# Performance work log

Measured on AMD Instinct MI355X. Metric: run time of the kernel, lower is better.

Reference implementation:

```python
import jax, jax.numpy as jnp
import numpy as np

B, S, D = 2, 2048, 2048
NQ, NKV = 32, 8
HD = D // NQ  # 64
THETA = 10000.0


def _rope_tables(seq_len, head_dim, theta):
    k = jnp.arange(0, head_dim, 2)[: head_dim // 2].astype(jnp.float32)
    inv_freq = 1.0 / (theta ** (k / head_dim))
    pos = jnp.arange(seq_len, dtype=jnp.float32)
    ang = pos[:, None] * inv_freq[None, :]          # [S, HD/2]
    ang = jnp.concatenate([ang, ang], axis=-1)       # [S, HD]
    return jnp.cos(ang), jnp.sin(ang)


def _apply_rope(x, cos, sin):
    # x: [B, H, S, HD]; cos/sin: [S, HD]
    h = x.shape[-1] // 2
    x1, x2 = x[..., :h], x[..., h:]
    rotated = jnp.concatenate([-x2, x1], axis=-1)
    return (x * cos[None, None] + rotated * sin[None, None]).astype(x.dtype)


def setup_inputs() -> dict:
    key = jax.random.key(0)
    ks = jax.random.split(key, 6)
    x = jax.random.normal(ks[0], (B, S, D), dtype=jnp.float32)
    attention_mask = jnp.ones((B, S), dtype=jnp.int32)
    Wq = jax.random.normal(ks[1], (NQ * HD, D), dtype=jnp.float32) * 0.02
    Wk = jax.random.normal(ks[2], (NKV * HD, D), dtype=jnp.float32) * 0.02
    Wv = jax.random.normal(ks[3], (NKV * HD, D), dtype=jnp.float32) * 0.02
    Wo = jax.random.normal(ks[4], (D, D), dtype=jnp.float32) * 0.02
    return {"x": x, "attention_mask": attention_mask,
            "Wq": Wq, "Wk": Wk, "Wv": Wv, "Wo": Wo}


def reference(x, attention_mask, Wq, Wk, Wv, Wo):
    b, s, d = x.shape
    # projections (nn.Linear: y = x @ W.T)
    q = jnp.einsum('bsd,od->bso', x, Wq).reshape(b, s, NQ, HD).transpose(0, 2, 1, 3)
    k = jnp.einsum('bsd,od->bso', x, Wk).reshape(b, s, NKV, HD).transpose(0, 2, 1, 3)
    v = jnp.einsum('bsd,od->bso', x, Wv).reshape(b, s, NKV, HD).transpose(0, 2, 1, 3)
    cos, sin = _rope_tables(s, HD, THETA)
    q = _apply_rope(q, cos, sin)
    k = _apply_rope(k, cos, sin)
    g = NQ // NKV
    k = jnp.repeat(k, g, axis=1)  # [b, NQ, s, HD]
    v = jnp.repeat(v, g, axis=1)
    attn = jnp.einsum('bhqd,bhkd->bhqk', q, k)
    causal = jnp.triu(jnp.ones((s, s), dtype=bool), k=1)
    attn = jnp.where(causal[None, None], -jnp.inf, attn)
    attn = jax.nn.softmax(attn / jnp.sqrt(jnp.float32(HD)), axis=-1)
    out = jnp.einsum('bhqk,bhkd->bhqd', attn, v)
    out = out.transpose(0, 2, 1, 3).reshape(b, s, d)
    return jnp.einsum('bsd,od->bso', out, Wo)
```

## Files before the change

kernel.cpp:

```cpp
#include <hip/hip_runtime.h>

#define B_   2
#define S_   2048
#define D_   2048
#define NQ_  32
#define NKV_ 8
#define HD_  64

typedef unsigned short u16;
typedef __bf16 bf16x8 __attribute__((ext_vector_type(8)));
typedef __bf16 bf16x4 __attribute__((ext_vector_type(4)));
typedef short  s16x4  __attribute__((ext_vector_type(4)));
typedef float  f32x4  __attribute__((ext_vector_type(4)));

#define GLB __attribute__((address_space(1)))
#define LDS __attribute__((address_space(3)))

__device__ inline u16 f2b(float f){
  union { float f; unsigned u; } v; v.f = f;
  unsigned r = (v.u + 0x7fffu + ((v.u >> 16) & 1u)) >> 16;
  return (u16)r;
}

__device__ inline f32x4 mfma16(bf16x4 a, bf16x4 b, f32x4 c){
  union U { bf16x4 b; s16x4 s; };
  U ua, ub; ua.b = a; ub.b = b;
  return __builtin_amdgcn_mfma_f32_16x16x16bf16_1k(ua.s, ub.s, c, 0, 0, 0);
}

__device__ inline bf16x4 pack4(float p0, float p1, float p2, float p3){
  union { float f; unsigned u; } a, b, c, d;
  a.f = p0; b.f = p1; c.f = p2; d.f = p3;
  union { uint2 u; bf16x4 v; } r;
  r.u.x = (a.u >> 16) | (b.u & 0xffff0000u);
  r.u.y = (c.u >> 16) | (d.u & 0xffff0000u);
  return r.v;
}

__global__ void k_f2b_all(const float* __restrict__ x,  const float* __restrict__ wq,
                          const float* __restrict__ wk, const float* __restrict__ wv,
                          const float* __restrict__ wo,
                          u16* __restrict__ xb, u16* __restrict__ wqkvb, u16* __restrict__ wob){
  int i = blockIdx.x * blockDim.x + threadIdx.x;
  const float* src; u16* dst; int off;
  if (i < 2097152)      { src = x;  dst = xb;                  off = i; }
  else if (i < 3145728) { src = wq; dst = wqkvb;               off = i - 2097152; }
  else if (i < 3407872) { src = wk; dst = wqkvb + 2048*2048;   off = i - 3145728; }
  else if (i < 3670016) { src = wv; dst = wqkvb + 2560*2048;   off = i - 3407872; }
  else                  { src = wo; dst = wob;                 off = i - 3670016; }
  float4 f = ((const float4*)src)[off];
  uint2 pk;
  pk.x = (unsigned)f2b(f.x) | ((unsigned)f2b(f.y) << 16);
  pk.y = (unsigned)f2b(f.z) | ((unsigned)f2b(f.w) << 16);
  ((uint2*)dst)[off] = pk;
}

#define GEMM_CORE(K)                                                           \
  __shared__ __align__(16) u16 As[128*64];                                     \
  __shared__ __align__(16) u16 Bs[128*64];                                     \
  const int tid  = threadIdx.x;                                               \
  const int lane = tid & 63;                                                  \
  const int wave = tid >> 6;                                                  \
  const int wm = wave >> 1, wn = wave & 1;                                    \
  const int quad = lane >> 4, l16 = lane & 15;                                \
  const u16* Ab = A  + (size_t)blockIdx.y * 128 * (K);                        \
  const u16* Bb = Bm + (size_t)blockIdx.x * 128 * (K);                        \
  f32x4 acc[4][4];                                                            \
  for (int i = 0; i < 4; i++)                                                 \
    for (int j = 0; j < 4; j++) acc[i][j] = (f32x4){0.f, 0.f, 0.f, 0.f};      \
  const int R0 = wave * 32;                                                   \
  const int lr = lane >> 3;                                                   \
  const int gc = ((lane & 7) ^ lr) * 8;                                       \
  const int sk = l16 & 7;                                                     \
  for (int k0 = 0; k0 < (K); k0 += 64){                                       \
    __syncthreads();                                                          \
    _Pragma("unroll")                                                         \
    for (int m = 0; m < 4; m++){                                              \
      const u16* ga = Ab + (size_t)(R0 + m*8 + lr) * (K) + k0 + gc;           \
      const u16* gb = Bb + (size_t)(R0 + m*8 + lr) * (K) + k0 + gc;           \
      __builtin_amdgcn_global_load_lds((const GLB void*)ga, (LDS void*)&As[(R0 + m*8)*64], 16, 0, 0); \
      __builtin_amdgcn_global_load_lds((const GLB void*)gb, (LDS void*)&Bs[(R0 + m*8)*64], 16, 0, 0); \
    }                                                                          \
    __syncthreads();                                                          \
    bf16x8 af[4][2], bfr[4][2];                                               \
    _Pragma("unroll")                                                         \
    for (int i = 0; i < 4; i++)                                               \
      _Pragma("unroll")                                                       \
      for (int h = 0; h < 2; h++)                                             \
        af[i][h]  = *(const bf16x8*)&As[(wm*64 + i*16 + l16)*64 + (((h*4 + quad) ^ sk)*8)]; \
    _Pragma("unroll")                                                         \
    for (int j = 0; j < 4; j++)                                               \
      _Pragma("unroll")                                                       \
      for (int h = 0; h < 2; h++)                                             \
        bfr[j][h] = *(const bf16x8*)&Bs[(wn*64 + j*16 + l16)*64 + (((h*4 + quad) ^ sk)*8)]; \
    _Pragma("unroll")                                                         \
    for (int i = 0; i < 4; i++)                                               \
      _Pragma("unroll")                                                       \
      for (int j = 0; j < 4; j++){                                            \
        acc[i][j] = __builtin_amdgcn_mfma_f32_16x16x32_bf16(af[i][0], bfr[j][0], acc[i][j], 0, 0, 0); \
        acc[i][j] = __builtin_amdgcn_mfma_f32_16x16x32_bf16(af[i][1], bfr[j][1], acc[i][j], 0, 0, 0); \
      }                                                                        \
  }

#define QSCALE 0.18033688011112042f
__global__ __launch_bounds__(256, 3) void k_gemm_qkv(const u16* __restrict__ A,
                                                     const u16* __restrict__ Bm,
                                                     u16* __restrict__ qT,
                                                     u16* __restrict__ kT,
                                                     u16* __restrict__ vT){
  GEMM_CORE(2048)

  const int cb = blockIdx.x*128 + wn*64;

  if (cb < 2560){
    const bool isq = (cb < 2048);
    const int hh   = (isq ? cb : (cb - 2048)) >> 6;
    const int NH   = isq ? NQ_ : NKV_;
    u16* base      = isq ? qT : kT;
    const float sc = isq ? QSCALE : 1.0f;
    #pragma unroll
    for (int j = 0; j < 2; j++){
      const int d2 = j*16 + l16;
      const float invf = __expf(-(float)d2 * (9.210340371976184f / 32.0f));
      #pragma unroll
      for (int i = 0; i < 4; i++){
        const int row0 = blockIdx.y*128 + wm*64 + i*16 + quad*4;
        #pragma unroll
        for (int r = 0; r < 4; r++){
          const int row = row0 + r;
          const int s = row & (S_ - 1), b = row >> 11;
          float ang = (float)s * invf;
          float sn = __sinf(ang), cs = __cosf(ang);
          const float x1 = acc[i][j][r] * sc, x2 = acc[i][j+2][r] * sc;
          u16* drow = base + ((size_t)(b*NH + hh) * S_ + s) * 64;
          drow[d2]      = f2b(x1*cs - x2*sn);
          drow[d2 + 32] = f2b(x2*cs + x1*sn);
        }
      }
    }
  } else {
    const int fbase = cb - 2560;
    #pragma unroll
    for (int j = 0; j < 4; j++){
      const int f = fbase + j*16 + l16;
      const int kvh = f >> 6, d = f & 63;
      #pragma unroll
      for (int i = 0; i < 4; i++){
        const int row0 = blockIdx.y*128 + wm*64 + i*16 + quad*4;
        const int s0 = row0 & (S_ - 1), b = row0 >> 11;
        uint2 pk;
        pk.x = (unsigned)f2b(acc[i][j][0]) | ((unsigned)f2b(acc[i][j][1]) << 16);
        pk.y = (unsigned)f2b(acc[i][j][2]) | ((unsigned)f2b(acc[i][j][3]) << 16);
        *(uint2*)(vT + ((size_t)(b*NKV_ + kvh) * 64 + d) * S_ + s0) = pk;
      }
    }
  }
}

__global__ __launch_bounds__(256, 3) void k_gemm_bt(const u16* __restrict__ A,
                                                    const u16* __restrict__ Bm,
                                                    float* __restrict__ C,
                                                    int N){
  GEMM_CORE(2048)
  for (int i = 0; i < 4; i++){
    int row0 = blockIdx.y*128 + wm*64 + i*16 + quad*4;
    for (int j = 0; j < 4; j++){
      int col = blockIdx.x*128 + wn*64 + j*16 + l16;
      for (int r = 0; r < 4; r++)
        C[(size_t)(row0 + r) * N + col] = acc[i][j][r];
    }
  }
}

__global__ __launch_bounds__(256) void k_attn(const u16* __restrict__ qT,
                                              const u16* __restrict__ kT,
                                              const u16* __restrict__ vT,
                                              u16* __restrict__ aout){
  __shared__ __align__(16) u16 Ks[2][64*64];
  __shared__ __align__(16) u16 Vs[2][64*64];

  const int bid = blockIdx.x;
  const int kvh = bid & 7;
  const int b   = (bid >> 3) & 1;
  const int hq  = (bid >> 4) & 3;
  const int T   = 15 - (bid >> 6);
  const int h   = kvh*4 + hq;
  const int lane = threadIdx.x & 63, w = threadIdx.x >> 6;
  const int quad = lane >> 4, l16 = lane & 15;

  const u16* Qh = qT + (size_t)(b*NQ_ + h)    * S_ * 64;
  const u16* Kh = kT + (size_t)(b*NKV_ + kvh) * S_ * 64;
  const u16* Vh = vT + (size_t)(b*NKV_ + kvh) * 64 * S_;

  const int rr = lane >> 3;
  const int gg = (lane & 7) ^ rr;
  const int R  = w * 16;

  auto stage = [&](int c, int buf){
    const int kb = c * 64;
    const u16* gk0 = Kh + (size_t)(kb + R + rr)     * 64 + gg*8;
    const u16* gk1 = Kh + (size_t)(kb + R + 8 + rr) * 64 + gg*8;
    const u16* gv0 = Vh + (size_t)(R + rr)     * S_ + kb + gg*8;
    const u16* gv1 = Vh + (size_t)(R + 8 + rr) * S_ + kb + gg*8;
    __builtin_amdgcn_global_load_lds((const GLB void*)gk0, (LDS void*)&Ks[buf][R*64],     16, 0, 0);
    __builtin_amdgcn_global_load_lds((const GLB void*)gk1, (LDS void*)&Ks[buf][(R+8)*64], 16, 0, 0);
    __builtin_amdgcn_global_load_lds((const GLB void*)gv0, (LDS void*)&Vs[buf][R*64],     16, 0, 0);
    __builtin_amdgcn_global_load_lds((const GLB void*)gv1, (LDS void*)&Vs[buf][(R+8)*64], 16, 0, 0);
  };

  const int sw    = l16 & 7;
  const int koff0 = ((quad    ) ^ sw) * 8;
  const int koff1 = ((quad + 4) ^ sw) * 8;
  int voff[4];
  #pragma unroll
  for (int t = 0; t < 4; t++)
    voff[t] = (((2*t + (quad >> 1)) ^ sw) * 8) + (quad & 1)*4;

  const int qb0 = 2*T, qb1 = 2*T + 1;
  const int qr0 = T*128 + w*16 + l16;
  const int qr1 = qr0 + 64;

  stage(0, 0);

  bf16x8 qf[2][2];
  qf[0][0] = *(const bf16x8*)(Qh + (size_t)qr0*64 + quad*8);
  qf[0][1] = *(const bf16x8*)(Qh + (size_t)qr0*64 + 32 + quad*8);
  qf[1][0] = *(const bf16x8*)(Qh + (size_t)qr1*64 + quad*8);
  qf[1][1] = *(const bf16x8*)(Qh + (size_t)qr1*64 + 32 + quad*8);

  f32x4 o[2][4];
  #pragma unroll
  for (int s = 0; s < 2; s++)
    for (int dt = 0; dt < 4; dt++) o[s][dt] = (f32x4){0.f, 0.f, 0.f, 0.f};
  float lrow[2] = {0.f, 0.f};

  for (int c = 0; c <= qb1; c++){
    const int buf = c & 1;
    __syncthreads();
    if (c < qb1) stage(c+1, buf^1);

    const bool act0  = (c <= qb0);
    const bool diag0 = (c == qb0);
    const bool diag1 = (c == qb1);
    const u16* Kb = &Ks[buf][0];
    const u16* Vb = &Vs[buf][0];

    bf16x4 pk[2][4];
    #pragma unroll
    for (int t = 0; t < 4; t++){
      const bool n0 = act0 && !(diag0 && t > w);
      const bool n1 = !(diag1 && t > w);
      if (!n0 && !n1) continue;
      const int rowb = (t*16 + l16)*64;
      bf16x8 ka0 = *(const bf16x8*)&Kb[rowb + koff0];
      bf16x8 ka1 = *(const bf16x8*)&Kb[rowb + koff1];
      #pragma unroll
      for (int s = 0; s < 2; s++){
        if (s == 0 ? !n0 : !n1) continue;
        f32x4 z = (f32x4){0.f, 0.f, 0.f, 0.f};
        z = __builtin_amdgcn_mfma_f32_16x16x32_bf16(ka0, qf[s][0], z, 0, 0, 0);
        z = __builtin_amdgcn_mfma_f32_16x16x32_bf16(ka1, qf[s][1], z, 0, 0, 0);
        if ((s == 0 ? diag0 : diag1) && t == w){
          #pragma unroll
          for (int r = 0; r < 4; r++)
            if (quad*4 + r > l16) z[r] = -1e30f;
        }
        float p0 = __builtin_amdgcn_exp2f(z[0]);
        float p1 = __builtin_amdgcn_exp2f(z[1]);
        float p2 = __builtin_amdgcn_exp2f(z[2]);
        float p3 = __builtin_amdgcn_exp2f(z[3]);
        lrow[s] += (p0 + p1) + (p2 + p3);
        pk[s][t] = pack4(p0, p1, p2, p3);
      }
    }

    #pragma unroll
    for (int dt = 0; dt < 4; dt++){
      const int rowb = (dt*16 + l16)*64;
      #pragma unroll
      for (int t = 0; t < 4; t++){
        const bool n0 = act0 && !(diag0 && t > w);
        const bool n1 = !(diag1 && t > w);
        if (!n0 && !n1) continue;
        bf16x4 va = *(const bf16x4*)&Vb[rowb + voff[t]];
        if (n0) o[0][dt] = mfma16(va, pk[0][t], o[0][dt]);
        if (n1) o[1][dt] = mfma16(va, pk[1][t], o[1][dt]);
      }
    }
  }

  #pragma unroll
  for (int s = 0; s < 2; s++){
    float lsum = lrow[s];
    lsum += __shfl_xor(lsum, 16, 64);
    lsum += __shfl_xor(lsum, 32, 64);
    float inv = 1.0f / lsum;
    const int qrow = s ? qr1 : qr0;
    u16* orow = aout + (size_t)(b*S_ + qrow) * D_ + h*64;
    #pragma unroll
    for (int dt = 0; dt < 4; dt++){
      uint2 pkd;
      u16 e0 = f2b(o[s][dt][0] * inv), e1 = f2b(o[s][dt][1] * inv);
      u16 e2 = f2b(o[s][dt][2] * inv), e3 = f2b(o[s][dt][3] * inv);
      pkd.x = (unsigned)e0 | ((unsigned)e1 << 16);
      pkd.y = (unsigned)e2 | ((unsigned)e3 << 16);
      *(uint2*)(orow + dt*16 + quad*4) = pkd;
    }
  }
}

extern "C" void kernel_launch(void* const* d_in, const int* in_sizes, int n_in,
                              void* d_out, int out_size, void* d_ws, size_t ws_size,
                              hipStream_t stream){
  const float* x  = (const float*)d_in[0];
  const float* Wq = (const float*)d_in[2];
  const float* Wk = (const float*)d_in[3];
  const float* Wv = (const float*)d_in[4];
  const float* Wo = (const float*)d_in[5];

  char* ws = (char*)d_ws;
  u16* xb    = (u16*)(ws);
  u16* wqkvb = (u16*)(ws + 16777216);
  u16* wob   = (u16*)(ws + 29360128);
  u16* qTp   = (u16*)(ws + 37748736);
  u16* kTp   = (u16*)(ws + 54525952);
  u16* vTp   = (u16*)(ws + 58720256);
  u16* attnOut = xb;

  k_f2b_all<<<dim3(18432), 256, 0, stream>>>(x, Wq, Wk, Wv, Wo, xb, wqkvb, wob);

  k_gemm_qkv<<<dim3(24, 32), 256, 0, stream>>>(xb, wqkvb, qTp, kTp, vTp);

  k_attn<<<dim3(1024), 256, 0, stream>>>(qTp, kTp, vTp, attnOut);

  k_gemm_bt<<<dim3(16, 32), 256, 0, stream>>>(attnOut, wob, (float*)d_out, 2048);
}
```

Baseline: 297.4 us.

## Split causal attention KV range across paired blocks and merge partials

Each attention block now handles two query tiles (p and 15-p), each over half of its KV range, so every block gets an equal amount of causal work. Unnormalized partial outputs and row sums go to two workspace buffers, and a new combine kernel sums them and normalizes. This removes the tail imbalance of the causal triangle but adds an extra kernel launch, extra global traffic for the bf16 partials, and an extra bf16 rounding step. It relies on the fixed-max exp2 trick (no running max), so partials can be added directly.

```diff
diff --git a/kernel.cpp b/kernel.cpp
--- a/kernel.cpp
+++ b/kernel.cpp
@@ -20,6 +20,10 @@
   union { float f; unsigned u; } v; v.f = f;
   unsigned r = (v.u + 0x7fffu + ((v.u >> 16) & 1u)) >> 16;
   return (u16)r;
+}
+__device__ inline float b2f(u16 b){
+  union { unsigned u; float f; } v; v.u = ((unsigned)b) << 16;
+  return v.f;
 }
 
 __device__ inline f32x4 mfma16(bf16x4 a, bf16x4 b, f32x4 c){
@@ -175,16 +179,20 @@
 __global__ __launch_bounds__(256) void k_attn(const u16* __restrict__ qT,
                                               const u16* __restrict__ kT,
                                               const u16* __restrict__ vT,
-                                              u16* __restrict__ aout){
+                                              u16* __restrict__ P1,
+                                              u16* __restrict__ P2,
+                                              float* __restrict__ l1,
+                                              float* __restrict__ l2){
   __shared__ __align__(16) u16 Ks[2][64*64];
   __shared__ __align__(16) u16 Vs[2][64*64];
 
-  const int bid = blockIdx.x;
-  const int kvh = bid & 7;
-  const int b   = (bid >> 3) & 1;
-  const int hq  = (bid >> 4) & 3;
-  const int T   = 15 - (bid >> 6);
-  const int h   = kvh*4 + hq;
+  const int bid  = blockIdx.x;
+  const int kvh  = bid & 7;
+  const int b    = (bid >> 3) & 1;
+  const int hq   = (bid >> 4) & 3;
+  const int p    = (bid >> 6) & 7;
+  const int half = bid >> 9;
+  const int h    = kvh*4 + hq;
   const int lane = threadIdx.x & 63, w = threadIdx.x >> 6;
   const int quad = lane >> 4, l16 = lane & 15;
 
@@ -216,97 +224,131 @@
   for (int t = 0; t < 4; t++)
     voff[t] = (((2*t + (quad >> 1)) ^ sw) * 8) + (quad & 1)*4;
 
-  const int qb0 = 2*T, qb1 = 2*T + 1;
-  const int qr0 = T*128 + w*16 + l16;
-  const int qr1 = qr0 + 64;
-
-  stage(0, 0);
-
-  bf16x8 qf[2][2];
-  qf[0][0] = *(const bf16x8*)(Qh + (size_t)qr0*64 + quad*8);
-  qf[0][1] = *(const bf16x8*)(Qh + (size_t)qr0*64 + 32 + quad*8);
-  qf[1][0] = *(const bf16x8*)(Qh + (size_t)qr1*64 + quad*8);
-  qf[1][1] = *(const bf16x8*)(Qh + (size_t)qr1*64 + 32 + quad*8);
-
-  f32x4 o[2][4];
-  #pragma unroll
-  for (int s = 0; s < 2; s++)
-    for (int dt = 0; dt < 4; dt++) o[s][dt] = (f32x4){0.f, 0.f, 0.f, 0.f};
-  float lrow[2] = {0.f, 0.f};
-
-  for (int c = 0; c <= qb1; c++){
-    const int buf = c & 1;
-    __syncthreads();
-    if (c < qb1) stage(c+1, buf^1);
-
-    const bool act0  = (c <= qb0);
-    const bool diag0 = (c == qb0);
-    const bool diag1 = (c == qb1);
-    const u16* Kb = &Ks[buf][0];
-    const u16* Vb = &Vs[buf][0];
-
-    bf16x4 pk[2][4];
+  for (int ph = 0; ph < 2; ph++){
+    int tile, c0, c1, slot;
+    if (ph == 0){ tile = p;
+      if (half == 0){ c0 = 0;      c1 = p + 1;     slot = 0; }
+      else          { c0 = p + 1;  c1 = 2*p + 2;   slot = 1; }
+    } else {      tile = 15 - p;
+      if (half == 0){ c0 = 16 - p; c1 = 32 - 2*p;  slot = 1; }
+      else          { c0 = 0;      c1 = 16 - p;    slot = 0; }
+    }
+    const int qb0 = 2*tile, qb1 = 2*tile + 1;
+    const int qr0 = tile*128 + w*16 + l16;
+    const int qr1 = qr0 + 64;
+    const int nc  = c1 - c0;
+
+    if (ph == 1) __syncthreads();
+    stage(c0, 0);
+
+    bf16x8 qf[2][2];
+    qf[0][0] = *(const bf16x8*)(Qh + (size_t)qr0*64 + quad*8);
+    qf[0][1] = *(const bf16x8*)(Qh + (size_t)qr0*64 + 32 + quad*8);
+    qf[1][0] = *(const bf16x8*)(Qh + (size_t)qr1*64 + quad*8);
+    qf[1][1] = *(const bf16x8*)(Qh + (size_t)qr1*64 + 32 + quad*8);
+
+    f32x4 o[2][4];
     #pragma unroll
-    for (int t = 0; t < 4; t++){
-      const bool n0 = act0 && !(diag0 && t > w);
-      const bool n1 = !(diag1 && t > w);
-      if (!n0 && !n1) continue;
-      const int rowb = (t*16 + l16)*64;
-      bf16x8 ka0 = *(const bf16x8*)&Kb[rowb + koff0];
-      bf16x8 ka1 = *(const bf16x8*)&Kb[rowb + koff1];
-      #pragma unroll
-      for (int s = 0; s < 2; s++){
-        if (s == 0 ? !n0 : !n1) continue;
-        f32x4 z = (f32x4){0.f, 0.f, 0.f, 0.f};
-        z = __builtin_amdgcn_mfma_f32_16x16x32_bf16(ka0, qf[s][0], z, 0, 0, 0);
-        z = __builtin_amdgcn_mfma_f32_16x16x32_bf16(ka1, qf[s][1], z, 0, 0, 0);
-        if ((s == 0 ? diag0 : diag1) && t == w){
-          #pragma unroll
-          for (int r = 0; r < 4; r++)
-            if (quad*4 + r > l16) z[r] = -1e30f;
-        }
-        float p0 = __builtin_amdgcn_exp2f(z[0]);
-        float p1 = __builtin_amdgcn_exp2f(z[1]);
-        float p2 = __builtin_amdgcn_exp2f(z[2]);
-        float p3 = __builtin_amdgcn_exp2f(z[3]);
-        lrow[s] += (p0 + p1) + (p2 + p3);
-        pk[s][t] = pack4(p0, p1, p2, p3);
-      }
-    }
-
-    #pragma unroll
-    for (int dt = 0; dt < 4; dt++){
-      const int rowb = (dt*16 + l16)*64;
+    for (int s = 0; s < 2; s++)
+      for (int dt = 0; dt < 4; dt++) o[s][dt] = (f32x4){0.f, 0.f, 0.f, 0.f};
+    float lrow[2] = {0.f, 0.f};
+
+    for (int i = 0; i < nc; i++){
+      const int c = c0 + i;
+      const int buf = i & 1;
+      __syncthreads();
+      if (i + 1 < nc) stage(c + 1, buf^1);
+
+      const bool act0  = (c <= qb0);
+      const bool diag0 = (c == qb0);
+      const bool diag1 = (c == qb1);
+      const u16* Kb = &Ks[buf][0];
+      const u16* Vb = &Vs[buf][0];
+
+      bf16x4 pk[2][4];
       #pragma unroll
       for (int t = 0; t < 4; t++){
         const bool n0 = act0 && !(diag0 && t > w);
         const bool n1 = !(diag1 && t > w);
         if (!n0 && !n1) continue;
-        bf16x4 va = *(const bf16x4*)&Vb[rowb + voff[t]];
-        if (n0) o[0][dt] = mfma16(va, pk[0][t], o[0][dt]);
-        if (n1) o[1][dt] = mfma16(va, pk[1][t], o[1][dt]);
+        const int rowb = (t*16 + l16)*64;
+        bf16x8 ka0 = *(const bf16x8*)&Kb[rowb + koff0];
+        bf16x8 ka1 = *(const bf16x8*)&Kb[rowb + koff1];
+        #pragma unroll
+        for (int s = 0; s < 2; s++){
+          if (s == 0 ? !n0 : !n1) continue;
+          f32x4 z = (f32x4){0.f, 0.f, 0.f, 0.f};
+          z = __builtin_amdgcn_mfma_f32_16x16x32_bf16(ka0, qf[s][0], z, 0, 0, 0);
+          z = __builtin_amdgcn_mfma_f32_16x16x32_bf16(ka1, qf[s][1], z, 0, 0, 0);
+          if ((s == 0 ? diag0 : diag1) && t == w){
+            #pragma unroll
+            for (int r = 0; r < 4; r++)
+              if (quad*4 + r > l16) z[r] = -1e30f;
+          }
+          float p0 = __builtin_amdgcn_exp2f(z[0]);
+          float p1 = __builtin_amdgcn_exp2f(z[1]);
+          float p2 = __builtin_amdgcn_exp2f(z[2]);
+          float p3 = __builtin_amdgcn_exp2f(z[3]);
+          lrow[s] += (p0 + p1) + (p2 + p3);
+          pk[s][t] = pack4(p0, p1, p2, p3);
+        }
+      }
+
+      #pragma unroll
+      for (int dt = 0; dt < 4; dt++){
+        const int rowb = (dt*16 + l16)*64;
+        #pragma unroll
+        for (int t = 0; t < 4; t++){
+          const bool n0 = act0 && !(diag0 && t > w);
+          const bool n1 = !(diag1 && t > w);
+          if (!n0 && !n1) continue;
+          bf16x4 va = *(const bf16x4*)&Vb[rowb + voff[t]];
+          if (n0) o[0][dt] = mfma16(va, pk[0][t], o[0][dt]);
+          if (n1) o[1][dt] = mfma16(va, pk[1][t], o[1][dt]);
+        }
+      }
+    }
+
+    u16*   Pd = slot ? P2 : P1;
+    float* ld = slot ? l2 : l1;
+    #pragma unroll
+    for (int s = 0; s < 2; s++){
+      float lsum = lrow[s];
+      lsum += __shfl_xor(lsum, 16, 64);
+      lsum += __shfl_xor(lsum, 32, 64);
+      const int qrow = s ? qr1 : qr0;
+      if (quad == 0) ld[(size_t)(b*S_ + qrow)*NQ_ + h] = lsum;
+      u16* orow = Pd + (size_t)(b*S_ + qrow) * D_ + h*64;
+      #pragma unroll
+      for (int dt = 0; dt < 4; dt++){
+        uint2 pkd;
+        u16 e0 = f2b(o[s][dt][0]), e1 = f2b(o[s][dt][1]);
+        u16 e2 = f2b(o[s][dt][2]), e3 = f2b(o[s][dt][3]);
+        pkd.x = (unsigned)e0 | ((unsigned)e1 << 16);
+        pkd.y = (unsigned)e2 | ((unsigned)e3 << 16);
+        *(uint2*)(orow + dt*16 + quad*4) = pkd;
       }
     }
   }
-
-  #pragma unroll
-  for (int s = 0; s < 2; s++){
-    float lsum = lrow[s];
-    lsum += __shfl_xor(lsum, 16, 64);
-    lsum += __shfl_xor(lsum, 32, 64);
-    float inv = 1.0f / lsum;
-    const int qrow = s ? qr1 : qr0;
-    u16* orow = aout + (size_t)(b*S_ + qrow) * D_ + h*64;
-    #pragma unroll
-    for (int dt = 0; dt < 4; dt++){
-      uint2 pkd;
-      u16 e0 = f2b(o[s][dt][0] * inv), e1 = f2b(o[s][dt][1] * inv);
-      u16 e2 = f2b(o[s][dt][2] * inv), e3 = f2b(o[s][dt][3] * inv);
-      pkd.x = (unsigned)e0 | ((unsigned)e1 << 16);
-      pkd.y = (unsigned)e2 | ((unsigned)e3 << 16);
-      *(uint2*)(orow + dt*16 + quad*4) = pkd;
-    }
-  }
+}
+
+__global__ void k_combine(const u16* __restrict__ P1, const u16* __restrict__ P2,
+                          const float* __restrict__ l1, const float* __restrict__ l2,
+                          u16* __restrict__ out){
+  int i = blockIdx.x * blockDim.x + threadIdx.x;
+  int e = i << 2;
+  int li = (e >> 11)*NQ_ + ((e >> 6) & 31);
+  float inv = 1.0f / (l1[li] + l2[li]);
+  uint2 a = *(const uint2*)(P1 + e);
+  uint2 bq = *(const uint2*)(P2 + e);
+  float o0 = (b2f(a.x & 0xffff)  + b2f(bq.x & 0xffff))  * inv;
+  float o1 = (b2f(a.x >> 16)     + b2f(bq.x >> 16))     * inv;
+  float o2 = (b2f(a.y & 0xffff)  + b2f(bq.y & 0xffff))  * inv;
+  float o3 = (b2f(a.y >> 16)     + b2f(bq.y >> 16))     * inv;
+  uint2 pk;
+  pk.x = (unsigned)f2b(o0) | ((unsigned)f2b(o1) << 16);
+  pk.y = (unsigned)f2b(o2) | ((unsigned)f2b(o3) << 16);
+  *(uint2*)(out + e) = pk;
 }
 
 extern "C" void kernel_launch(void* const* d_in, const int* in_sizes, int n_in,
@@ -319,19 +361,25 @@
   const float* Wo = (const float*)d_in[5];
 
   char* ws = (char*)d_ws;
-  u16* xb    = (u16*)(ws);
-  u16* wqkvb = (u16*)(ws + 16777216);
-  u16* wob   = (u16*)(ws + 29360128);
-  u16* qTp   = (u16*)(ws + 37748736);
-  u16* kTp   = (u16*)(ws + 54525952);
-  u16* vTp   = (u16*)(ws + 58720256);
-  u16* attnOut = xb;
+  u16*   xb    = (u16*)(ws);
+  u16*   wqkvb = (u16*)(ws + 16777216);
+  u16*   wob   = (u16*)(ws + 29360128);
+  u16*   qTp   = (u16*)(ws + 37748736);
+  u16*   kTp   = (u16*)(ws + 54525952);
+  u16*   vTp   = (u16*)(ws + 58720256);
+  u16*   P1    = xb;
+  u16*   P2    = (u16*)(ws + 62914560);
+  float* l1    = (float*)(ws + 79691776);
+  float* l2    = (float*)(ws + 80216064);
+  u16*   attnOut = qTp;
 
   k_f2b_all<<<dim3(18432), 256, 0, stream>>>(x, Wq, Wk, Wv, Wo, xb, wqkvb, wob);
 
   k_gemm_qkv<<<dim3(24, 32), 256, 0, stream>>>(xb, wqkvb, qTp, kTp, vTp);
 
-  k_attn<<<dim3(1024), 256, 0, stream>>>(qTp, kTp, vTp, attnOut);
+  k_attn<<<dim3(1024), 256, 0, stream>>>(qTp, kTp, vTp, P1, P2, l1, l2);
+
+  k_combine<<<dim3(8192), 256, 0, stream>>>(P1, P2, l1, l2, attnOut);
 
   k_gemm_bt<<<dim3(16, 32), 256, 0, stream>>>(attnOut, wob, (float*)d_out, 2048);
 }
```

Measured after the change: 309.7 us. +4.1%, slower.
